# Performance work log

Hardware: AMD Instinct MI355X
Metric: run time of the kernel (lower is better)

## Reference

```python
import jax, jax.numpy as jnp
import numpy as np

N_T, N_M, E, Q = 100000, 20000, 600000, 200000
F_IN, D, L = 256, 128, 2


def setup_inputs() -> dict:
    key = jax.random.key(0)
    ks = jax.random.split(key, 20)
    s = 1.0 / np.sqrt(D)
    inp = {
        "x_thesis": jax.random.normal(ks[0], (N_T, F_IN), jnp.float32),
        "mentor_node_id": jnp.arange(N_M, dtype=jnp.int64) if jax.config.jax_enable_x64 else jnp.arange(N_M, dtype=jnp.int32),
        "edge_src": jax.random.randint(ks[1], (E,), 0, N_T),
        "edge_dst": jax.random.randint(ks[2], (E,), 0, N_M),
        "eli_src": jax.random.randint(ks[3], (Q,), 0, N_T),
        "eli_dst": jax.random.randint(ks[4], (Q,), 0, N_M),
        # encoder params
        "thesis_lin_w": jax.random.normal(ks[5], (D, F_IN), jnp.float32) / np.sqrt(F_IN),
        "thesis_lin_b": jnp.zeros((D,), jnp.float32),
        "prof_emb": jax.random.normal(ks[6], (N_M, D), jnp.float32),
        # SAGEConv params per layer, per edge type (sup: thesis->mentor, rev: mentor->thesis)
        "W_nbr_sup": jax.random.normal(ks[7], (L, D, D), jnp.float32) * s,
        "W_root_sup": jax.random.normal(ks[8], (L, D, D), jnp.float32) * s,
        "b_sup": jnp.zeros((L, D), jnp.float32),
        "W_nbr_rev": jax.random.normal(ks[9], (L, D, D), jnp.float32) * s,
        "W_root_rev": jax.random.normal(ks[10], (L, D, D), jnp.float32) * s,
        "b_rev": jnp.zeros((L, D), jnp.float32),
        # classifier Linear(2*D -> 1)
        "cls_w": jax.random.normal(ks[11], (2 * D,), jnp.float32) * (1.0 / np.sqrt(2 * D)),
        "cls_b": jnp.zeros((), jnp.float32),
    }
    return inp


def reference(x_thesis, mentor_node_id, edge_src, edge_dst, eli_src, eli_dst,
              thesis_lin_w, thesis_lin_b, prof_emb,
              W_nbr_sup, W_root_sup, b_sup, W_nbr_rev, W_root_rev, b_rev,
              cls_w, cls_b):
    n_t = x_thesis.shape[0]
    n_m = prof_emb.shape[0]
    L_ = W_nbr_sup.shape[0]

    # node encoders
    h_t = x_thesis @ thesis_lin_w.T + thesis_lin_b          # [N_T, D]
    h_m = prof_emb[mentor_node_id]                          # [N_M, D]

    ones = jnp.ones(edge_src.shape[0], h_t.dtype)
    deg_m = jnp.maximum(jax.ops.segment_sum(ones, edge_dst, num_segments=n_m), 1.0)[:, None]
    deg_t = jnp.maximum(jax.ops.segment_sum(ones, edge_src, num_segments=n_t), 1.0)[:, None]

    for l in range(L_):
        # mean-aggregate thesis feats onto mentors (supervised_by edges)
        agg_m = jax.ops.segment_sum(h_t[edge_src], edge_dst, num_segments=n_m) / deg_m
        # mean-aggregate mentor feats onto theses (reverse edges)
        agg_t = jax.ops.segment_sum(h_m[edge_dst], edge_src, num_segments=n_t) / deg_t
        new_m = agg_m @ W_nbr_sup[l].T + h_m @ W_root_sup[l].T + b_sup[l]
        new_t = agg_t @ W_nbr_rev[l].T + h_t @ W_root_rev[l].T + b_rev[l]
        if l < L_ - 1:
            new_m = jax.nn.relu(new_m)
            new_t = jax.nn.relu(new_t)
        h_t, h_m = new_t, new_m

    # edge-level classifier: gather endpoints, concat, linear -> scalar per pair
    z = jnp.concatenate([h_t[eli_src], h_m[eli_dst]], axis=-1)  # [Q, 2D]
    return z @ cls_w + cls_b                                     # [Q]
```

## Files before the change

kernel.cpp:

```cpp
#include <hip/hip_runtime.h>
#include <cstdint>
#include <cstddef>

#define D 128
#define F_IN 256

typedef __attribute__((ext_vector_type(8))) short bf16x8;
typedef __attribute__((ext_vector_type(4))) float f32x4;

__device__ __forceinline__ unsigned short f2bs(float f) {
  unsigned int x = __builtin_bit_cast(unsigned int, f);
  x = x + 0x7fffu + ((x >> 16) & 1u);
  return (unsigned short)(x >> 16);
}
__device__ __forceinline__ float b2f(unsigned int lo16) {
  unsigned int x = lo16 << 16;
  return __builtin_bit_cast(float, x);
}
__device__ __forceinline__ void gl_lds16v(const void* g, void* l) {
  __builtin_amdgcn_global_load_lds(
      (__attribute__((address_space(1))) void*)g,
      (__attribute__((address_space(3))) void*)l, 16, 0, 0);
}
__device__ __forceinline__ uint4 pack8(float4 a, float4 b) {
  uint4 o;
  o.x = (unsigned)f2bs(a.x) | ((unsigned)f2bs(a.y) << 16);
  o.y = (unsigned)f2bs(a.z) | ((unsigned)f2bs(a.w) << 16);
  o.z = (unsigned)f2bs(b.x) | ((unsigned)f2bs(b.y) << 16);
  o.w = (unsigned)f2bs(b.z) | ((unsigned)f2bs(b.w) << 16);
  return o;
}


__global__ __launch_bounds__(256) void prep_k(
    const float* __restrict__ s0, unsigned short* __restrict__ d0, int n0,
    const float* __restrict__ s1, unsigned short* __restrict__ d1, int n1,
    const float* __restrict__ s2, unsigned short* __restrict__ d2, int n2,
    const float* __restrict__ s3, unsigned short* __restrict__ d3, int n3,
    const float* __restrict__ s4, unsigned short* __restrict__ d4, int n4,
    int nbC,
    const float* __restrict__ emb, const int* __restrict__ ids,
    unsigned short* __restrict__ hm, int NM, int nbG,
    const int* __restrict__ esrc, const int* __restrict__ edst,
    int* __restrict__ bktT, int* __restrict__ bktM,
    int E, int SHT, int SHM, int nbA)
{
  int bid = blockIdx.x;
  int tid = threadIdx.x;
  if (bid < nbC) {
    int j = bid * 256 + tid;
    const float* s; unsigned short* d;
    if (j < n0) { s = s0; d = d0; }
    else {
      j -= n0;
      if (j < n1) { s = s1; d = d1; }
      else {
        j -= n1;
        if (j < n2) { s = s2; d = d2; }
        else {
          j -= n2;
          if (j < n3) { s = s3; d = d3; }
          else { j -= n3; if (j >= n4) return; s = s4; d = d4; }
        }
      }
    }
    const float4* sp = (const float4*)(s + (size_t)j * 8);
    *(uint4*)(d + (size_t)j * 8) = pack8(sp[0], sp[1]);
    return;
  }
  bid -= nbC;
  if (bid < nbG) {
    int i = bid * 256 + tid;
    if (i >= NM * 16) return;
    int r = i >> 4, c = (i & 15) * 8;
    const float* s = emb + (size_t)ids[r] * D + c;
    *(uint4*)(hm + (size_t)r * D + c) = pack8(*(const float4*)s, *(const float4*)(s + 4));
    return;
  }
  bid -= nbG;
  __shared__ int sh[256];
  sh[tid] = 0;
  __syncthreads();
  int stride = nbA * 256;
  for (int e = bid * 256 + tid; e < E; e += stride) {
    atomicAdd(&sh[esrc[e] >> SHT], 1);
    atomicAdd(&sh[128 + (edst[e] >> SHM)], 1);
  }
  __syncthreads();
  if (tid < 128) { if (sh[tid]) atomicAdd(&bktT[tid], sh[tid]); }
  else { if (sh[tid]) atomicAdd(&bktM[tid - 128], sh[tid]); }
}


__global__ void a2_scan_k(const int* __restrict__ bktT, int* __restrict__ baseT, int* __restrict__ curT, int BT,
                          const int* __restrict__ bktM, int* __restrict__ baseM, int* __restrict__ curM, int BM) {
  __shared__ int sT[129], sM[129];
  int tid = threadIdx.x;
  if (tid < BT) sT[tid] = bktT[tid];
  if (tid < BM) sM[tid] = bktM[tid];
  __syncthreads();
  if (tid == 0) { int r = 0; for (int i = 0; i < BT; ++i) { int c = sT[i]; sT[i] = r; r += c; } sT[BT] = r; }
  if (tid == 1) { int r = 0; for (int i = 0; i < BM; ++i) { int c = sM[i]; sM[i] = r; r += c; } sM[BM] = r; }
  __syncthreads();
  if (tid <= BT) { baseT[tid] = sT[tid]; if (tid < BT) curT[tid] = sT[tid]; }
  if (tid <= BM) { baseM[tid] = sM[tid]; if (tid < BM) curM[tid] = sM[tid]; }
}


#define CH 4096

__global__ __launch_bounds__(256) void a3_part_k(
    const int* __restrict__ esrc, const int* __restrict__ edst,
    unsigned* __restrict__ partT, unsigned* __restrict__ partM,
    int* __restrict__ curT, int* __restrict__ curM,
    int E, int BT, int BM, int SHT, int SHM)
{
  __shared__ unsigned stT[CH], stM[CH];
  __shared__ int hT[128], lbT[128], lcT[128], gbT[128];
  __shared__ int hM[128], lbM[128], lcM[128], gbM[128];
  __shared__ int st2[256];
  int tid = threadIdx.x;
  int c0 = blockIdx.x * CH;
  int len = E - c0; if (len > CH) len = CH;

  if (tid < 128) { hT[tid] = 0; hM[tid] = 0; }
  __syncthreads();
  for (int i = tid; i < len; i += 256) {
    atomicAdd(&hT[esrc[c0 + i] >> SHT], 1);
    atomicAdd(&hM[edst[c0 + i] >> SHM], 1);
  }
  __syncthreads();
  int own = (tid < 128) ? hT[tid] : hM[tid - 128];
  st2[tid] = own;
  __syncthreads();
  for (int dd = 1; dd < 128; dd <<= 1) {
    int y = ((tid & 127) >= dd) ? st2[tid - dd] : 0;
    __syncthreads();
    st2[tid] += y;
    __syncthreads();
  }
  int excl = st2[tid] - own;
  if (tid < 128) { lbT[tid] = excl; lcT[tid] = excl; }
  else { lbM[tid - 128] = excl; lcM[tid - 128] = excl; }
  __syncthreads();
  if (tid < BT) { if (hT[tid]) gbT[tid] = atomicAdd(&curT[tid], hT[tid]); }
  if (tid >= 128 && tid - 128 < BM) { int m = tid - 128; if (hM[m]) gbM[m] = atomicAdd(&curM[m], hM[m]); }
  __syncthreads();
  for (int i = tid; i < len; i += 256) {
    unsigned s = (unsigned)esrc[c0 + i], dn = (unsigned)edst[c0 + i];
    int p = atomicAdd(&lcT[s >> SHT], 1);
    stT[p] = (s << 15) | dn;
    int q = atomicAdd(&lcM[dn >> SHM], 1);
    stM[q] = (dn << 17) | s;
  }
  __syncthreads();
  for (int b = 0; b < BT; ++b) {
    int cb = hT[b]; if (!cb) continue;
    int lb = lbT[b]; int gb = gbT[b];
    for (int i = tid; i < cb; i += 256) partT[gb + i] = stT[lb + i];
  }
  for (int b = 0; b < BM; ++b) {
    int cb = hM[b]; if (!cb) continue;
    int lb = lbM[b]; int gb = gbM[b];
    for (int i = tid; i < cb; i += 256) partM[gb + i] = stM[lb + i];
  }
}


#define BCAP 12288

__global__ __launch_bounds__(256) void b_csr_k(
    const unsigned* __restrict__ partT, const int* __restrict__ baseT,
    int* __restrict__ rowT, int* __restrict__ csrT, int NT, int BT, int SHT,
    const unsigned* __restrict__ partM, const int* __restrict__ baseM,
    int* __restrict__ rowM, int* __restrict__ csrM, int NM, int BM, int SHM, int E)
{
  __shared__ int cnt[1024];
  __shared__ int st[256];
  __shared__ unsigned stage[BCAP];

  const unsigned* part; const int* base; int* row; int* csr;
  int N, SH, KS; unsigned PM; int b; bool last;
  if ((int)blockIdx.x < BT) {
    part = partT; base = baseT; row = rowT; csr = csrT;
    N = NT; SH = SHT; KS = 15; PM = 0x7fffu; b = blockIdx.x; last = (b == BT - 1);
  } else {
    part = partM; base = baseM; row = rowM; csr = csrM;
    N = NM; SH = SHM; KS = 17; PM = 0x1ffffu; b = blockIdx.x - BT; last = (b == BM - 1);
  }
  int tid = threadIdx.x;
  int ebeg = base[b], eend = base[b + 1];
  int tot = eend - ebeg;
  int n0 = b << SH;
  int width = 1 << SH;
  int nw = N - n0; if (nw > width) nw = width;
  int seg = (width + 255) >> 8;

  for (int j = 0; j < seg; ++j) { int idx = tid * seg + j; if (idx < nw) cnt[idx] = 0; }
  __syncthreads();
  for (int i = tid; i < tot; i += 256) {
    int k = (int)(part[ebeg + i] >> KS) - n0;
    atomicAdd(&cnt[k], 1);
  }
  __syncthreads();
  int s = 0;
  for (int j = 0; j < seg; ++j) { int idx = tid * seg + j; if (idx < nw) s += cnt[idx]; }
  st[tid] = s;
  __syncthreads();
  for (int dd = 1; dd < 256; dd <<= 1) {
    int y = (tid >= dd) ? st[tid - dd] : 0;
    __syncthreads();
    st[tid] += y;
    __syncthreads();
  }
  int run = st[tid] - s;
  for (int j = 0; j < seg; ++j) {
    int idx = tid * seg + j;
    if (idx < nw) {
      int c = cnt[idx];
      row[n0 + idx] = ebeg + run;
      cnt[idx] = run;
      run += c;
    }
  }
  if (last && tid == 0) row[N] = E;
  __syncthreads();
  if (tot <= BCAP) {
    for (int i = tid; i < tot; i += 256) {
      unsigned p = part[ebeg + i];
      int k = (int)(p >> KS) - n0;
      int pos = atomicAdd(&cnt[k], 1);
      stage[pos] = p & PM;
    }
    __syncthreads();
    for (int i = tid; i < tot; i += 256) csr[ebeg + i] = (int)stage[i];
  } else {
    for (int i = tid; i < tot; i += 256) {
      unsigned p = part[ebeg + i];
      int k = (int)(p >> KS) - n0;
      int pos = atomicAdd(&cnt[k], 1);
      csr[ebeg + pos] = (int)(p & PM);
    }
  }
}


__global__ __launch_bounds__(256) void aggregate2_k(
    const unsigned short* __restrict__ tabM, const int* __restrict__ rowpM,
    const int* __restrict__ idxM, unsigned short* __restrict__ outM, int nM, int nblkM,
    const unsigned short* __restrict__ tabT, const int* __restrict__ rowpT,
    const int* __restrict__ idxT, unsigned short* __restrict__ outT, int nT)
{
  const unsigned short* tab; const int* rowp; const int* idx;
  unsigned short* outp; int n, nodeb;
  if ((int)blockIdx.x < nblkM) {
    tab = tabM; rowp = rowpM; idx = idxM; outp = outM; n = nM;
    nodeb = blockIdx.x * 8;
  } else {
    tab = tabT; rowp = rowpT; idx = idxT; outp = outT; n = nT;
    nodeb = (blockIdx.x - nblkM) * 8;
  }
  const int tid = threadIdx.x;
  const int l = tid & 63;
  const int l32 = l & 31;
  const int sub = l >> 5;
  const int node = nodeb + (tid >> 6) * 2 + sub;
  const int nodeC = node < n ? node : n - 1;
  int b = rowp[nodeC];
  int e = rowp[nodeC + 1];
  if (node >= n) e = b;
  const int deg = e - b;
  const int odeg = __shfl_xor(deg, 32, 64);
  const int trip = deg > odeg ? deg : odeg;
  const int qsafe = (e > b) ? (e - 1) : 0;
  const unsigned short* tl = tab + l32 * 4;
  float a0 = 0.f, a1 = 0.f, a2 = 0.f, a3 = 0.f;
  int k = 0;
  while (k + 8 <= trip) {
    int nn[8]; bool ok[8];
#pragma unroll
    for (int u = 0; u < 8; ++u) { int p = b + k + u; ok[u] = p < e; nn[u] = idx[ok[u] ? p : qsafe]; }
    uint2 vv[8];
#pragma unroll
    for (int u = 0; u < 8; ++u) { vv[u] = make_uint2(0u, 0u); if (ok[u]) vv[u] = *(const uint2*)(tl + (size_t)nn[u] * D); }
#pragma unroll
    for (int u = 0; u < 8; ++u) {
      a0 += b2f(vv[u].x & 0xffffu); a1 += b2f(vv[u].x >> 16);
      a2 += b2f(vv[u].y & 0xffffu); a3 += b2f(vv[u].y >> 16);
    }
    k += 8;
  }
  if (k + 4 <= trip) {
    int nn[4]; bool ok[4];
#pragma unroll
    for (int u = 0; u < 4; ++u) { int p = b + k + u; ok[u] = p < e; nn[u] = idx[ok[u] ? p : qsafe]; }
    uint2 vv[4];
#pragma unroll
    for (int u = 0; u < 4; ++u) { vv[u] = make_uint2(0u, 0u); if (ok[u]) vv[u] = *(const uint2*)(tl + (size_t)nn[u] * D); }
#pragma unroll
    for (int u = 0; u < 4; ++u) {
      a0 += b2f(vv[u].x & 0xffffu); a1 += b2f(vv[u].x >> 16);
      a2 += b2f(vv[u].y & 0xffffu); a3 += b2f(vv[u].y >> 16);
    }
    k += 4;
  }
  if (k < trip) {
    int nn[3]; bool ok[3];
#pragma unroll
    for (int u = 0; u < 3; ++u) { int p = b + k + u; ok[u] = p < e; nn[u] = idx[ok[u] ? p : qsafe]; }
    uint2 vv[3];
#pragma unroll
    for (int u = 0; u < 3; ++u) { vv[u] = make_uint2(0u, 0u); if (ok[u]) vv[u] = *(const uint2*)(tl + (size_t)nn[u] * D); }
#pragma unroll
    for (int u = 0; u < 3; ++u) {
      a0 += b2f(vv[u].x & 0xffffu); a1 += b2f(vv[u].x >> 16);
      a2 += b2f(vv[u].y & 0xffffu); a3 += b2f(vv[u].y >> 16);
    }
  }
  float inv = 1.0f / (float)(deg > 1 ? deg : 1);
  if (node < n) {
    uint2 o;
    o.x = (unsigned)f2bs(a0 * inv) | ((unsigned)f2bs(a1 * inv) << 16);
    o.y = (unsigned)f2bs(a2 * inv) | ((unsigned)f2bs(a3 * inv) << 16);
    *(uint2*)(outp + (size_t)node * D + l32 * 4) = o;
  }
}


template<bool RELU>
__device__ __forceinline__ void gemm_body(
    const unsigned short* __restrict__ Aop, const unsigned short* __restrict__ WA,
    const unsigned short* __restrict__ Bop, const unsigned short* __restrict__ WB,
    const float* __restrict__ bias, unsigned short* __restrict__ out, int M,
    int blk, char* smraw)
{
  unsigned short* bufA0 = (unsigned short*)smraw;
  unsigned short* bufW0 = (unsigned short*)(smraw + 16384);
  const int tid = threadIdx.x;
  const int w = tid >> 6, l = tid & 63;
  const int wr = w >> 1, wc = w & 1;
  const int lr = l & 15, kg = l >> 4;
  const int row0 = blk * 128;
  const int srow = l >> 2;
  const int su = l & 3;

  f32x4 acc[4][4] = {};

  auto stage = [&](int st, int bsel) {
    const unsigned short* Ap = (st < 4) ? Aop : Bop;
    const unsigned short* Wp = (st < 4) ? WA : WB;
    int k0 = (st & 3) * 32;
    unsigned short* bA = bufA0 + bsel * 4096;
    unsigned short* bW = bufW0 + bsel * 4096;
#pragma unroll
    for (int q = 0; q < 2; ++q) {
      int r = w * 32 + q * 16 + srow;
      int gr = row0 + r; if (gr >= M) gr = M - 1;
      int gu = su ^ ((r >> 1) & 3);
      gl_lds16v(Ap + (size_t)gr * D + k0 + gu * 8, bA + (w * 32 + q * 16) * 32 + l * 8);
      gl_lds16v(Wp + (size_t)r * D + k0 + gu * 8, bW + (w * 32 + q * 16) * 32 + l * 8);
    }
  };

  stage(0, 0);
#pragma unroll 1
  for (int st = 0; st < 8; ++st) {
    if (st < 7) {
      stage(st + 1, (st + 1) & 1);
      __builtin_amdgcn_sched_barrier(0);
      asm volatile("s_waitcnt vmcnt(4)" ::: "memory");
    } else {
      __builtin_amdgcn_sched_barrier(0);
      asm volatile("s_waitcnt vmcnt(0)" ::: "memory");
    }
    __builtin_amdgcn_s_barrier();
    __builtin_amdgcn_sched_barrier(0);
    const unsigned short* bA = bufA0 + (st & 1) * 4096;
    const unsigned short* bW = bufW0 + (st & 1) * 4096;
    bf16x8 aF[4], bF[4];
#pragma unroll
    for (int i = 0; i < 4; ++i) {
      int r = wr * 64 + i * 16 + lr;
      aF[i] = *(const bf16x8*)&bA[r * 32 + ((kg ^ ((r >> 1) & 3)) * 8)];
    }
#pragma unroll
    for (int j = 0; j < 4; ++j) {
      int r = wc * 64 + j * 16 + lr;
      bF[j] = *(const bf16x8*)&bW[r * 32 + ((kg ^ ((r >> 1) & 3)) * 8)];
    }
#pragma unroll
    for (int i = 0; i < 4; ++i)
#pragma unroll
      for (int j = 0; j < 4; ++j)
        acc[i][j] = __builtin_amdgcn_mfma_f32_16x16x32_bf16(aF[i], bF[j], acc[i][j], 0, 0, 0);
    __builtin_amdgcn_sched_barrier(0);
    __builtin_amdgcn_s_barrier();
  }

  __syncthreads();
  float bn[4];
#pragma unroll
  for (int j = 0; j < 4; ++j) bn[j] = bias[wc * 64 + j * 16 + lr];
  unsigned short* ow = (unsigned short*)smraw + w * 4096;
#pragma unroll
  for (int i = 0; i < 4; ++i)
#pragma unroll
    for (int j = 0; j < 4; ++j) {
      f32x4 v = acc[i][j];
#pragma unroll
      for (int r = 0; r < 4; ++r) {
        float x = v[r] + bn[j];
        if (RELU) x = fmaxf(x, 0.f);
        ow[(i * 16 + kg * 4 + r) * 64 + j * 16 + lr] = f2bs(x);
      }
    }
  __syncthreads();
#pragma unroll
  for (int q = 0; q < 8; ++q) {
    int u = q * 64 + l;
    int lrow = u >> 3;
    int cu = (u & 7) * 8;
    int gr = row0 + wr * 64 + lrow;
    if (gr < M)
      *(uint4*)(out + (size_t)gr * D + wc * 64 + cu) = *(const uint4*)&ow[lrow * 64 + cu];
  }
}

template<bool RELU>
__global__ __launch_bounds__(256) void gemm_pair_k(
    const unsigned short* __restrict__ Am, const unsigned short* __restrict__ WAm,
    const unsigned short* __restrict__ Bm, const unsigned short* __restrict__ WBm,
    const float* __restrict__ biasm, unsigned short* __restrict__ outm, int Mm, int nbm,
    const unsigned short* __restrict__ At, const unsigned short* __restrict__ WAt,
    const unsigned short* __restrict__ Bt, const unsigned short* __restrict__ WBt,
    const float* __restrict__ biast, unsigned short* __restrict__ outt, int Mt)
{
  __shared__ char smraw[32768];
  if ((int)blockIdx.x < nbm)
    gemm_body<RELU>(Am, WAm, Bm, WBm, biasm, outm, Mm, blockIdx.x, smraw);
  else
    gemm_body<RELU>(At, WAt, Bt, WBt, biast, outt, Mt, blockIdx.x - nbm, smraw);
}

__global__ __launch_bounds__(256) void gemm_enc_k(
    const float* __restrict__ A, const unsigned short* __restrict__ W,
    const float* __restrict__ bias, unsigned short* __restrict__ out, int M)
{
  __shared__ char smraw[49152];
  float* bufA0 = (float*)smraw;
  unsigned short* bufW0 = (unsigned short*)(smraw + 32768);
  const int tid = threadIdx.x;
  const int w = tid >> 6, l = tid & 63;
  const int wr = w >> 1, wc = w & 1;
  const int lr = l & 15, kg = l >> 4;
  const int row0 = blockIdx.x * 128;
  const int arow = l >> 3;
  const int au = l & 7;
  const int wrow = l >> 2;
  const int wu = l & 3;

  f32x4 acc[4][4] = {};

  auto stage = [&](int st, int bsel) {
    int k0 = st * 32;
    float* bA = bufA0 + bsel * 4096;
    unsigned short* bW = bufW0 + bsel * 4096;
#pragma unroll
    for (int q = 0; q < 4; ++q) {
      int r = w * 32 + q * 8 + arow;
      int gr = row0 + r; if (gr >= M) gr = M - 1;
      int gu = au ^ (r & 7);
      gl_lds16v(A + (size_t)gr * F_IN + k0 + gu * 4, bA + (w * 32 + q * 8) * 32 + l * 4);
    }
#pragma unroll
    for (int q = 0; q < 2; ++q) {
      int r = w * 32 + q * 16 + wrow;
      int gu = wu ^ ((r >> 1) & 3);
      gl_lds16v(W + (size_t)r * F_IN + k0 + gu * 8, bW + (w * 32 + q * 16) * 32 + l * 8);
    }
  };

  stage(0, 0);
#pragma unroll 1
  for (int st = 0; st < F_IN / 32; ++st) {
    if (st < F_IN / 32 - 1) {
      stage(st + 1, (st + 1) & 1);
      __builtin_amdgcn_sched_barrier(0);
      asm volatile("s_waitcnt vmcnt(6)" ::: "memory");
    } else {
      __builtin_amdgcn_sched_barrier(0);
      asm volatile("s_waitcnt vmcnt(0)" ::: "memory");
    }
    __builtin_amdgcn_s_barrier();
    __builtin_amdgcn_sched_barrier(0);
    const float* bA = bufA0 + (st & 1) * 4096;
    const unsigned short* bW = bufW0 + (st & 1) * 4096;
    bf16x8 aF[4], bF[4];
#pragma unroll
    for (int i = 0; i < 4; ++i) {
      int r = wr * 64 + i * 16 + lr;
      const float4* pa = (const float4*)(bA + r * 32);
      float4 v0 = pa[(2 * kg) ^ (r & 7)];
      float4 v1 = pa[(2 * kg + 1) ^ (r & 7)];
      uint4 c = pack8(v0, v1);
      aF[i] = *(bf16x8*)&c;
    }
#pragma unroll
    for (int j = 0; j < 4; ++j) {
      int r = wc * 64 + j * 16 + lr;
      bF[j] = *(const bf16x8*)&bW[r * 32 + ((kg ^ ((r >> 1) & 3)) * 8)];
    }
#pragma unroll
    for (int i = 0; i < 4; ++i)
#pragma unroll
      for (int j = 0; j < 4; ++j)
        acc[i][j] = __builtin_amdgcn_mfma_f32_16x16x32_bf16(aF[i], bF[j], acc[i][j], 0, 0, 0);
    __builtin_amdgcn_sched_barrier(0);
    __builtin_amdgcn_s_barrier();
  }

  __syncthreads();
  float bn[4];
#pragma unroll
  for (int j = 0; j < 4; ++j) bn[j] = bias[wc * 64 + j * 16 + lr];
  unsigned short* ow = (unsigned short*)smraw + w * 4096;
#pragma unroll
  for (int i = 0; i < 4; ++i)
#pragma unroll
    for (int j = 0; j < 4; ++j) {
      f32x4 v = acc[i][j];
#pragma unroll
      for (int r = 0; r < 4; ++r)
        ow[(i * 16 + kg * 4 + r) * 64 + j * 16 + lr] = f2bs(v[r] + bn[j]);
    }
  __syncthreads();
#pragma unroll
  for (int q = 0; q < 8; ++q) {
    int u = q * 64 + l;
    int lrow = u >> 3;
    int cu = (u & 7) * 8;
    int gr = row0 + wr * 64 + lrow;
    if (gr < M)
      *(uint4*)(out + (size_t)gr * D + wc * 64 + cu) = *(const uint4*)&ow[lrow * 64 + cu];
  }
}


__global__ __launch_bounds__(256) void classify_k(
    const unsigned short* __restrict__ ht, const unsigned short* __restrict__ hm,
    const int* __restrict__ qs, const int* __restrict__ qd,
    const float* __restrict__ w, const float* __restrict__ bptr,
    float* __restrict__ out, int Q)
{
  int g = blockIdx.x * 8 + (threadIdx.x >> 5);
  if (g >= Q) return;
  int l = threadIdx.x & 31;
  const unsigned short* src = (l < 16)
      ? ht + (size_t)qs[g] * D + l * 8
      : hm + (size_t)qd[g] * D + (l - 16) * 8;
  uint4 v = *(const uint4*)src;
  const float* wp = w + l * 8;
  float acc = 0.f;
  acc += b2f(v.x & 0xffffu) * wp[0];
  acc += b2f(v.x >> 16)     * wp[1];
  acc += b2f(v.y & 0xffffu) * wp[2];
  acc += b2f(v.y >> 16)     * wp[3];
  acc += b2f(v.z & 0xffffu) * wp[4];
  acc += b2f(v.z >> 16)     * wp[5];
  acc += b2f(v.w & 0xffffu) * wp[6];
  acc += b2f(v.w >> 16)     * wp[7];
#pragma unroll
  for (int m = 16; m >= 1; m >>= 1) acc += __shfl_xor(acc, m, 64);
  if (l == 0) out[g] = acc + bptr[0];
}


extern "C" void kernel_launch(void* const* d_in, const int* in_sizes, int n_in,
                              void* d_out, int out_size, void* d_ws, size_t ws_size,
                              hipStream_t stream)
{
  const float* x_thesis = (const float*)d_in[0];
  const int*   mentor_id = (const int*)d_in[1];
  const int*   esrc = (const int*)d_in[2];
  const int*   edst = (const int*)d_in[3];
  const int*   qsrc = (const int*)d_in[4];
  const int*   qdst = (const int*)d_in[5];
  const float* lin_w = (const float*)d_in[6];
  const float* lin_b = (const float*)d_in[7];
  const float* prof  = (const float*)d_in[8];
  const float* Wn_sup = (const float*)d_in[9];
  const float* Wr_sup = (const float*)d_in[10];
  const float* b_sup  = (const float*)d_in[11];
  const float* Wn_rev = (const float*)d_in[12];
  const float* Wr_rev = (const float*)d_in[13];
  const float* b_rev  = (const float*)d_in[14];
  const float* cls_w  = (const float*)d_in[15];
  const float* cls_b  = (const float*)d_in[16];

  const int NT = in_sizes[0] / F_IN;
  const int NM = in_sizes[1];
  const int E  = in_sizes[2];
  const int Q  = in_sizes[4];
  const int L  = in_sizes[11] / D;

  int SHT = 0; while ((((NT - 1) >> SHT) + 1) > 128) ++SHT;
  int SHM = 0; while ((((NM - 1) >> SHM) + 1) > 128) ++SHM;
  const int BT = ((NT - 1) >> SHT) + 1;
  const int BM = ((NM - 1) >> SHM) + 1;

  char* wsb = (char*)d_ws;
  size_t off = 0;
  auto alloc = [&](size_t bytes) {
    void* p = wsb + off;
    off = (off + bytes + 255) & ~(size_t)255;
    return p;
  };
  unsigned short* h_t   = (unsigned short*)alloc((size_t)NT * D * 2);
  unsigned short* a_t   = (unsigned short*)alloc((size_t)NT * D * 2);
  unsigned short* h_m   = (unsigned short*)alloc((size_t)NM * D * 2);
  unsigned short* a_m   = (unsigned short*)alloc((size_t)NM * D * 2);
  unsigned short* linw_bf = (unsigned short*)alloc((size_t)D * F_IN * 2);
  unsigned short* wns_bf  = (unsigned short*)alloc((size_t)L * D * D * 2);
  unsigned short* wrs_bf  = (unsigned short*)alloc((size_t)L * D * D * 2);
  unsigned short* wnr_bf  = (unsigned short*)alloc((size_t)L * D * D * 2);
  unsigned short* wrr_bf  = (unsigned short*)alloc((size_t)L * D * D * 2);
  int* row_t = (int*)alloc(((size_t)NT + 1) * 4);
  int* row_m = (int*)alloc(((size_t)NM + 1) * 4);
  int* csr_t = (int*)alloc((size_t)E * 4);
  int* csr_m = (int*)alloc((size_t)E * 4);
  unsigned* partT = (unsigned*)alloc((size_t)E * 4);
  unsigned* partM = (unsigned*)alloc((size_t)E * 4);
  size_t bkt_off = off;
  int* bktT  = (int*)alloc(128 * 4);
  int* bktM  = (int*)alloc(128 * 4);
  size_t bkt_end = off;
  int* baseT = (int*)alloc(129 * 4);
  int* baseM = (int*)alloc(129 * 4);
  int* curT  = (int*)alloc(128 * 4);
  int* curM  = (int*)alloc(128 * 4);
  (void)n_in; (void)out_size; (void)ws_size;

  (void)hipMemsetAsync(wsb + bkt_off, 0, bkt_end - bkt_off, stream);

  {
    int n0 = D * F_IN / 8, nw = L * D * D / 8;
    int totc = n0 + 4 * nw;
    int nbC = (totc + 255) / 256;
    int nbG = (NM * 16 + 255) / 256;
    int nbA = 256;
    prep_k<<<nbC + nbG + nbA, 256, 0, stream>>>(
        lin_w, linw_bf, n0, Wn_sup, wns_bf, nw, Wr_sup, wrs_bf, nw,
        Wn_rev, wnr_bf, nw, Wr_rev, wrr_bf, nw, nbC,
        prof, mentor_id, h_m, NM, nbG,
        esrc, edst, bktT, bktM, E, SHT, SHM, nbA);
  }
  a2_scan_k<<<1, 256, 0, stream>>>(bktT, baseT, curT, BT, bktM, baseM, curM, BM);
  a3_part_k<<<(E + CH - 1) / CH, 256, 0, stream>>>(
      esrc, edst, partT, partM, curT, curM, E, BT, BM, SHT, SHM);
  b_csr_k<<<BT + BM, 256, 0, stream>>>(
      partT, baseT, row_t, csr_t, NT, BT, SHT,
      partM, baseM, row_m, csr_m, NM, BM, SHM, E);

  gemm_enc_k<<<(NT + 127) / 128, 256, 0, stream>>>(x_thesis, linw_bf, lin_b, h_t, NT);

  int agg_nbm = (NM + 7) / 8, agg_nbt = (NT + 7) / 8;
  int gem_nbm = (NM + 127) / 128, gem_nbt = (NT + 127) / 128;
  for (int l = 0; l < L; ++l) {
    aggregate2_k<<<agg_nbm + agg_nbt, 256, 0, stream>>>(
        h_t, row_m, csr_m, a_m, NM, agg_nbm,
        h_m, row_t, csr_t, a_t, NT);

    const unsigned short* wns = wns_bf + (size_t)l * D * D;
    const unsigned short* wrs = wrs_bf + (size_t)l * D * D;
    const unsigned short* wnr = wnr_bf + (size_t)l * D * D;
    const unsigned short* wrr = wrr_bf + (size_t)l * D * D;
    const float* bs = b_sup + (size_t)l * D;
    const float* br = b_rev + (size_t)l * D;
    if (l < L - 1) {
      gemm_pair_k<true><<<gem_nbm + gem_nbt, 256, 0, stream>>>(
          a_m, wns, h_m, wrs, bs, a_m, NM, gem_nbm,
          a_t, wnr, h_t, wrr, br, a_t, NT);
    } else {
      gemm_pair_k<false><<<gem_nbm + gem_nbt, 256, 0, stream>>>(
          a_m, wns, h_m, wrs, bs, a_m, NM, gem_nbm,
          a_t, wnr, h_t, wrr, br, a_t, NT);
    }
    unsigned short* tmp;
    tmp = h_t; h_t = a_t; a_t = tmp;
    tmp = h_m; h_m = a_m; a_m = tmp;
  }

  classify_k<<<(Q + 7) / 8, 256, 0, stream>>>(h_t, h_m, qsrc, qdst, cls_w, cls_b,
                                              (float*)d_out, Q);
}
```

Before: 270.6 us.

## Fuse edge partition with encoder GEMM and widen aggregate gathers to 16B

Merges the edge-partition kernel and the thesis encoder GEMM into one launch, with block ranges dispatched to each body over a shared LDS buffer. Independent work can then overlap and one launch disappears. The aggregation kernel now has each half-wave of 16 lanes gather 16-byte rows, with even and odd neighbours split across halves and combined by a shuffle, instead of 32 lanes loading 8 bytes. This issues fewer, wider memory requests, but raises register use and adds masked work for low-degree nodes.

New measurement: 256.8 us. 1.05x faster.

```diff
diff --git a/kernel.cpp b/kernel.cpp
--- a/kernel.cpp
+++ b/kernel.cpp
@@ -13,6 +13,9 @@
   x = x + 0x7fffu + ((x >> 16) & 1u);
   return (unsigned short)(x >> 16);
 }
+__device__ __forceinline__ unsigned pk2(float lo, float hi) {
+  return (unsigned)f2bs(lo) | ((unsigned)f2bs(hi) << 16);
+}
 __device__ __forceinline__ float b2f(unsigned int lo16) {
   unsigned int x = lo16 << 16;
   return __builtin_bit_cast(float, x);
@@ -24,10 +27,8 @@
 }
 __device__ __forceinline__ uint4 pack8(float4 a, float4 b) {
   uint4 o;
-  o.x = (unsigned)f2bs(a.x) | ((unsigned)f2bs(a.y) << 16);
-  o.y = (unsigned)f2bs(a.z) | ((unsigned)f2bs(a.w) << 16);
-  o.z = (unsigned)f2bs(b.x) | ((unsigned)f2bs(b.y) << 16);
-  o.w = (unsigned)f2bs(b.z) | ((unsigned)f2bs(b.w) << 16);
+  o.x = pk2(a.x, a.y); o.y = pk2(a.z, a.w);
+  o.z = pk2(b.x, b.y); o.w = pk2(b.z, b.w);
   return o;
 }
 
@@ -109,18 +110,26 @@
 
 #define CH 4096
 
-__global__ __launch_bounds__(256) void a3_part_k(
+__device__ __forceinline__ void a3_body(
     const int* __restrict__ esrc, const int* __restrict__ edst,
     unsigned* __restrict__ partT, unsigned* __restrict__ partM,
     int* __restrict__ curT, int* __restrict__ curM,
-    int E, int BT, int BM, int SHT, int SHM)
-{
-  __shared__ unsigned stT[CH], stM[CH];
-  __shared__ int hT[128], lbT[128], lcT[128], gbT[128];
-  __shared__ int hM[128], lbM[128], lcM[128], gbM[128];
-  __shared__ int st2[256];
+    int E, int BT, int BM, int SHT, int SHM, int blk, char* smraw)
+{
+  unsigned* stT = (unsigned*)smraw;
+  unsigned* stM = stT + CH;
+  int* hT  = (int*)(stM + CH);
+  int* lbT = hT + 128;
+  int* lcT = hT + 256;
+  int* gbT = hT + 384;
+  int* hM  = hT + 512;
+  int* lbM = hT + 640;
+  int* lcM = hT + 768;
+  int* gbM = hT + 896;
+  int* st2 = hT + 1024;
+
   int tid = threadIdx.x;
-  int c0 = blockIdx.x * CH;
+  int c0 = blk * CH;
   int len = E - c0; if (len > CH) len = CH;
 
   if (tid < 128) { hT[tid] = 0; hM[tid] = 0; }
@@ -164,6 +173,125 @@
     int lb = lbM[b]; int gb = gbM[b];
     for (int i = tid; i < cb; i += 256) partM[gb + i] = stM[lb + i];
   }
+}
+
+
+__device__ __forceinline__ void enc_body(
+    const float* __restrict__ A, const unsigned short* __restrict__ W,
+    const float* __restrict__ bias, unsigned short* __restrict__ out, int M,
+    int blk, char* smraw)
+{
+  float* bufA0 = (float*)smraw;
+  unsigned short* bufW0 = (unsigned short*)(smraw + 32768);
+  const int tid = threadIdx.x;
+  const int w = tid >> 6, l = tid & 63;
+  const int wr = w >> 1, wc = w & 1;
+  const int lr = l & 15, kg = l >> 4;
+  const int row0 = blk * 128;
+  const int arow = l >> 3;
+  const int au = l & 7;
+  const int wrow = l >> 2;
+  const int wu = l & 3;
+
+  f32x4 acc[4][4] = {};
+
+  auto stage = [&](int st, int bsel) {
+    int k0 = st * 32;
+    float* bA = bufA0 + bsel * 4096;
+    unsigned short* bW = bufW0 + bsel * 4096;
+#pragma unroll
+    for (int q = 0; q < 4; ++q) {
+      int r = w * 32 + q * 8 + arow;
+      int gr = row0 + r; if (gr >= M) gr = M - 1;
+      int gu = au ^ (r & 7);
+      gl_lds16v(A + (size_t)gr * F_IN + k0 + gu * 4, bA + (w * 32 + q * 8) * 32 + l * 4);
+    }
+#pragma unroll
+    for (int q = 0; q < 2; ++q) {
+      int r = w * 32 + q * 16 + wrow;
+      int gu = wu ^ ((r >> 1) & 3);
+      gl_lds16v(W + (size_t)r * F_IN + k0 + gu * 8, bW + (w * 32 + q * 16) * 32 + l * 8);
+    }
+  };
+
+  stage(0, 0);
+#pragma unroll 1
+  for (int st = 0; st < F_IN / 32; ++st) {
+    if (st < F_IN / 32 - 1) {
+      stage(st + 1, (st + 1) & 1);
+      __builtin_amdgcn_sched_barrier(0);
+      asm volatile("s_waitcnt vmcnt(6)" ::: "memory");
+    } else {
+      __builtin_amdgcn_sched_barrier(0);
+      asm volatile("s_waitcnt vmcnt(0)" ::: "memory");
+    }
+    __builtin_amdgcn_s_barrier();
+    __builtin_amdgcn_sched_barrier(0);
+    const float* bA = bufA0 + (st & 1) * 4096;
+    const unsigned short* bW = bufW0 + (st & 1) * 4096;
+    bf16x8 aF[4], bF[4];
+#pragma unroll
+    for (int i = 0; i < 4; ++i) {
+      int r = wr * 64 + i * 16 + lr;
+      const float4* pa = (const float4*)(bA + r * 32);
+      float4 v0 = pa[(2 * kg) ^ (r & 7)];
+      float4 v1 = pa[(2 * kg + 1) ^ (r & 7)];
+      uint4 c = pack8(v0, v1);
+      aF[i] = *(bf16x8*)&c;
+    }
+#pragma unroll
+    for (int j = 0; j < 4; ++j) {
+      int r = wc * 64 + j * 16 + lr;
+      bF[j] = *(const bf16x8*)&bW[r * 32 + ((kg ^ ((r >> 1) & 3)) * 8)];
+    }
+#pragma unroll
+    for (int i = 0; i < 4; ++i)
+#pragma unroll
+      for (int j = 0; j < 4; ++j)
+        acc[i][j] = __builtin_amdgcn_mfma_f32_16x16x32_bf16(aF[i], bF[j], acc[i][j], 0, 0, 0);
+    __builtin_amdgcn_sched_barrier(0);
+    __builtin_amdgcn_s_barrier();
+  }
+
+  __syncthreads();
+  float bn[4];
+#pragma unroll
+  for (int j = 0; j < 4; ++j) bn[j] = bias[wc * 64 + j * 16 + lr];
+  unsigned short* ow = (unsigned short*)smraw + w * 4096;
+#pragma unroll
+  for (int i = 0; i < 4; ++i)
+#pragma unroll
+    for (int j = 0; j < 4; ++j) {
+      f32x4 v = acc[i][j];
+#pragma unroll
+      for (int r = 0; r < 4; ++r)
+        ow[(i * 16 + kg * 4 + r) * 64 + j * 16 + lr] = f2bs(v[r] + bn[j]);
+    }
+  __syncthreads();
+#pragma unroll
+  for (int q = 0; q < 8; ++q) {
+    int u = q * 64 + l;
+    int lrow = u >> 3;
+    int cu = (u & 7) * 8;
+    int gr = row0 + wr * 64 + lrow;
+    if (gr < M)
+      *(uint4*)(out + (size_t)gr * D + wc * 64 + cu) = *(const uint4*)&ow[lrow * 64 + cu];
+  }
+}
+
+__global__ __launch_bounds__(256) void a3enc_k(
+    const int* __restrict__ esrc, const int* __restrict__ edst,
+    unsigned* __restrict__ partT, unsigned* __restrict__ partM,
+    int* __restrict__ curT, int* __restrict__ curM,
+    int E, int BT, int BM, int SHT, int SHM, int nbA3,
+    const float* __restrict__ A, const unsigned short* __restrict__ W,
+    const float* __restrict__ bias, unsigned short* __restrict__ out, int M)
+{
+  __shared__ char smraw[49152];
+  if ((int)blockIdx.x < nbA3)
+    a3_body(esrc, edst, partT, partM, curT, curM, E, BT, BM, SHT, SHM, blockIdx.x, smraw);
+  else
+    enc_body(A, W, bias, out, M, blockIdx.x - nbA3, smraw);
 }
 
 
@@ -245,7 +373,7 @@
 }
 
 
-__global__ __launch_bounds__(256) void aggregate2_k(
+__global__ __launch_bounds__(256) void aggregate3_k(
     const unsigned short* __restrict__ tabM, const int* __restrict__ rowpM,
     const int* __restrict__ idxM, unsigned short* __restrict__ outM, int nM, int nblkM,
     const unsigned short* __restrict__ tabT, const int* __restrict__ rowpT,
@@ -262,67 +390,62 @@
   }
   const int tid = threadIdx.x;
   const int l = tid & 63;
-  const int l32 = l & 31;
   const int sub = l >> 5;
+  const int half = (l >> 4) & 1;
+  const int l16 = l & 15;
   const int node = nodeb + (tid >> 6) * 2 + sub;
   const int nodeC = node < n ? node : n - 1;
   int b = rowp[nodeC];
   int e = rowp[nodeC + 1];
   if (node >= n) e = b;
   const int deg = e - b;
-  const int odeg = __shfl_xor(deg, 32, 64);
-  const int trip = deg > odeg ? deg : odeg;
-  const int qsafe = (e > b) ? (e - 1) : 0;
-  const unsigned short* tl = tab + l32 * 4;
+  int nb = (deg + 15) >> 4;
+  int onb = __shfl_xor(nb, 32, 64);
+  int trip = nb > onb ? nb : onb;
+  const unsigned short* tl = tab + l16 * 8;
+
   float a0 = 0.f, a1 = 0.f, a2 = 0.f, a3 = 0.f;
-  int k = 0;
-  while (k + 8 <= trip) {
-    int nn[8]; bool ok[8];
-#pragma unroll
-    for (int u = 0; u < 8; ++u) { int p = b + k + u; ok[u] = p < e; nn[u] = idx[ok[u] ? p : qsafe]; }
-    uint2 vv[8];
-#pragma unroll
-    for (int u = 0; u < 8; ++u) { vv[u] = make_uint2(0u, 0u); if (ok[u]) vv[u] = *(const uint2*)(tl + (size_t)nn[u] * D); }
+  float a4 = 0.f, a5 = 0.f, a6 = 0.f, a7 = 0.f;
+  for (int t = 0; t < trip; ++t) {
+    int base = b + t * 16 + half;
+    int pp[8]; bool ok[8];
+#pragma unroll
+    for (int u = 0; u < 8; ++u) {
+      int p = base + 2 * u;
+      ok[u] = p < e;
+      pp[u] = ok[u] ? idx[p] : 0;
+    }
+    uint4 vv[8];
+#pragma unroll
+    for (int u = 0; u < 8; ++u) {
+      uint4 z; z.x = 0u; z.y = 0u; z.z = 0u; z.w = 0u;
+      vv[u] = z;
+      if (ok[u]) vv[u] = *(const uint4*)(tl + (size_t)pp[u] * D);
+    }
 #pragma unroll
     for (int u = 0; u < 8; ++u) {
       a0 += b2f(vv[u].x & 0xffffu); a1 += b2f(vv[u].x >> 16);
       a2 += b2f(vv[u].y & 0xffffu); a3 += b2f(vv[u].y >> 16);
-    }
-    k += 8;
-  }
-  if (k + 4 <= trip) {
-    int nn[4]; bool ok[4];
-#pragma unroll
-    for (int u = 0; u < 4; ++u) { int p = b + k + u; ok[u] = p < e; nn[u] = idx[ok[u] ? p : qsafe]; }
-    uint2 vv[4];
-#pragma unroll
-    for (int u = 0; u < 4; ++u) { vv[u] = make_uint2(0u, 0u); if (ok[u]) vv[u] = *(const uint2*)(tl + (size_t)nn[u] * D); }
-#pragma unroll
-    for (int u = 0; u < 4; ++u) {
-      a0 += b2f(vv[u].x & 0xffffu); a1 += b2f(vv[u].x >> 16);
-      a2 += b2f(vv[u].y & 0xffffu); a3 += b2f(vv[u].y >> 16);
-    }
-    k += 4;
-  }
-  if (k < trip) {
-    int nn[3]; bool ok[3];
-#pragma unroll
-    for (int u = 0; u < 3; ++u) { int p = b + k + u; ok[u] = p < e; nn[u] = idx[ok[u] ? p : qsafe]; }
-    uint2 vv[3];
-#pragma unroll
-    for (int u = 0; u < 3; ++u) { vv[u] = make_uint2(0u, 0u); if (ok[u]) vv[u] = *(const uint2*)(tl + (size_t)nn[u] * D); }
-#pragma unroll
-    for (int u = 0; u < 3; ++u) {
-      a0 += b2f(vv[u].x & 0xffffu); a1 += b2f(vv[u].x >> 16);
-      a2 += b2f(vv[u].y & 0xffffu); a3 += b2f(vv[u].y >> 16);
-    }
-  }
-  float inv = 1.0f / (float)(deg > 1 ? deg : 1);
-  if (node < n) {
-    uint2 o;
-    o.x = (unsigned)f2bs(a0 * inv) | ((unsigned)f2bs(a1 * inv) << 16);
-    o.y = (unsigned)f2bs(a2 * inv) | ((unsigned)f2bs(a3 * inv) << 16);
-    *(uint2*)(outp + (size_t)node * D + l32 * 4) = o;
+      a4 += b2f(vv[u].z & 0xffffu); a5 += b2f(vv[u].z >> 16);
+      a6 += b2f(vv[u].w & 0xffffu); a7 += b2f(vv[u].w >> 16);
+    }
+  }
+  a0 += __shfl_xor(a0, 16, 64);
+  a1 += __shfl_xor(a1, 16, 64);
+  a2 += __shfl_xor(a2, 16, 64);
+  a3 += __shfl_xor(a3, 16, 64);
+  a4 += __shfl_xor(a4, 16, 64);
+  a5 += __shfl_xor(a5, 16, 64);
+  a6 += __shfl_xor(a6, 16, 64);
+  a7 += __shfl_xor(a7, 16, 64);
+  if (node < n && half == 0) {
+    float inv = 1.0f / (float)(deg > 1 ? deg : 1);
+    uint4 o;
+    o.x = pk2(a0 * inv, a1 * inv);
+    o.y = pk2(a2 * inv, a3 * inv);
+    o.z = pk2(a4 * inv, a5 * inv);
+    o.w = pk2(a6 * inv, a7 * inv);
+    *(uint4*)(outp + (size_t)node * D + l16 * 8) = o;
   }
 }
 
@@ -440,109 +563,6 @@
     gemm_body<RELU>(Am, WAm, Bm, WBm, biasm, outm, Mm, blockIdx.x, smraw);
   else
     gemm_body<RELU>(At, WAt, Bt, WBt, biast, outt, Mt, blockIdx.x - nbm, smraw);
-}
-
-__global__ __launch_bounds__(256) void gemm_enc_k(
-    const float* __restrict__ A, const unsigned short* __restrict__ W,
-    const float* __restrict__ bias, unsigned short* __restrict__ out, int M)
-{
-  __shared__ char smraw[49152];
-  float* bufA0 = (float*)smraw;
-  unsigned short* bufW0 = (unsigned short*)(smraw + 32768);
-  const int tid = threadIdx.x;
-  const int w = tid >> 6, l = tid & 63;
-  const int wr = w >> 1, wc = w & 1;
-  const int lr = l & 15, kg = l >> 4;
-  const int row0 = blockIdx.x * 128;
-  const int arow = l >> 3;
-  const int au = l & 7;
-  const int wrow = l >> 2;
-  const int wu = l & 3;
-
-  f32x4 acc[4][4] = {};
-
-  auto stage = [&](int st, int bsel) {
-    int k0 = st * 32;
-    float* bA = bufA0 + bsel * 4096;
-    unsigned short* bW = bufW0 + bsel * 4096;
-#pragma unroll
-    for (int q = 0; q < 4; ++q) {
-      int r = w * 32 + q * 8 + arow;
-      int gr = row0 + r; if (gr >= M) gr = M - 1;
-      int gu = au ^ (r & 7);
-      gl_lds16v(A + (size_t)gr * F_IN + k0 + gu * 4, bA + (w * 32 + q * 8) * 32 + l * 4);
-    }
-#pragma unroll
-    for (int q = 0; q < 2; ++q) {
-      int r = w * 32 + q * 16 + wrow;
-      int gu = wu ^ ((r >> 1) & 3);
-      gl_lds16v(W + (size_t)r * F_IN + k0 + gu * 8, bW + (w * 32 + q * 16) * 32 + l * 8);
-    }
-  };
-
-  stage(0, 0);
-#pragma unroll 1
-  for (int st = 0; st < F_IN / 32; ++st) {
-    if (st < F_IN / 32 - 1) {
-      stage(st + 1, (st + 1) & 1);
-      __builtin_amdgcn_sched_barrier(0);
-      asm volatile("s_waitcnt vmcnt(6)" ::: "memory");
-    } else {
-      __builtin_amdgcn_sched_barrier(0);
-      asm volatile("s_waitcnt vmcnt(0)" ::: "memory");
-    }
-    __builtin_amdgcn_s_barrier();
-    __builtin_amdgcn_sched_barrier(0);
-    const float* bA = bufA0 + (st & 1) * 4096;
-    const unsigned short* bW = bufW0 + (st & 1) * 4096;
-    bf16x8 aF[4], bF[4];
-#pragma unroll
-    for (int i = 0; i < 4; ++i) {
-      int r = wr * 64 + i * 16 + lr;
-      const float4* pa = (const float4*)(bA + r * 32);
-      float4 v0 = pa[(2 * kg) ^ (r & 7)];
-      float4 v1 = pa[(2 * kg + 1) ^ (r & 7)];
-      uint4 c = pack8(v0, v1);
-      aF[i] = *(bf16x8*)&c;
-    }
-#pragma unroll
-    for (int j = 0; j < 4; ++j) {
-      int r = wc * 64 + j * 16 + lr;
-      bF[j] = *(const bf16x8*)&bW[r * 32 + ((kg ^ ((r >> 1) & 3)) * 8)];
-    }
-#pragma unroll
-    for (int i = 0; i < 4; ++i)
-#pragma unroll
-      for (int j = 0; j < 4; ++j)
-        acc[i][j] = __builtin_amdgcn_mfma_f32_16x16x32_bf16(aF[i], bF[j], acc[i][j], 0, 0, 0);
-    __builtin_amdgcn_sched_barrier(0);
-    __builtin_amdgcn_s_barrier();
-  }
-
-  __syncthreads();
-  float bn[4];
-#pragma unroll
-  for (int j = 0; j < 4; ++j) bn[j] = bias[wc * 64 + j * 16 + lr];
-  unsigned short* ow = (unsigned short*)smraw + w * 4096;
-#pragma unroll
-  for (int i = 0; i < 4; ++i)
-#pragma unroll
-    for (int j = 0; j < 4; ++j) {
-      f32x4 v = acc[i][j];
-#pragma unroll
-      for (int r = 0; r < 4; ++r)
-        ow[(i * 16 + kg * 4 + r) * 64 + j * 16 + lr] = f2bs(v[r] + bn[j]);
-    }
-  __syncthreads();
-#pragma unroll
-  for (int q = 0; q < 8; ++q) {
-    int u = q * 64 + l;
-    int lrow = u >> 3;
-    int cu = (u & 7) * 8;
-    int gr = row0 + wr * 64 + lrow;
-    if (gr < M)
-      *(uint4*)(out + (size_t)gr * D + wc * 64 + cu) = *(const uint4*)&ow[lrow * 64 + cu];
-  }
 }
 
 
@@ -655,18 +675,21 @@
         esrc, edst, bktT, bktM, E, SHT, SHM, nbA);
   }
   a2_scan_k<<<1, 256, 0, stream>>>(bktT, baseT, curT, BT, bktM, baseM, curM, BM);
-  a3_part_k<<<(E + CH - 1) / CH, 256, 0, stream>>>(
-      esrc, edst, partT, partM, curT, curM, E, BT, BM, SHT, SHM);
+
+  int nbA3 = (E + CH - 1) / CH;
+  int nbEnc = (NT + 127) / 128;
+  a3enc_k<<<nbA3 + nbEnc, 256, 0, stream>>>(
+      esrc, edst, partT, partM, curT, curM, E, BT, BM, SHT, SHM, nbA3,
+      x_thesis, linw_bf, lin_b, h_t, NT);
+
   b_csr_k<<<BT + BM, 256, 0, stream>>>(
       partT, baseT, row_t, csr_t, NT, BT, SHT,
       partM, baseM, row_m, csr_m, NM, BM, SHM, E);
 
-  gemm_enc_k<<<(NT + 127) / 128, 256, 0, stream>>>(x_thesis, linw_bf, lin_b, h_t, NT);
-
   int agg_nbm = (NM + 7) / 8, agg_nbt = (NT + 7) / 8;
   int gem_nbm = (NM + 127) / 128, gem_nbt = (NT + 127) / 128;
   for (int l = 0; l < L; ++l) {
-    aggregate2_k<<<agg_nbm + agg_nbt, 256, 0, stream>>>(
+    aggregate3_k<<<agg_nbm + agg_nbt, 256, 0, stream>>>(
         h_t, row_m, csr_m, a_m, NM, agg_nbm,
         h_m, row_t, csr_t, a_t, NT);
 
```
